# Kernel optimization log

Hardware: AMD Instinct MI355X
Metric: run time of the kernel (lower is better)

## Reference

```python
import jax, jax.numpy as jnp
import numpy as np

B, N, C = 64, 1700, 256
E_SP, E_TM = 6400, 10000


def gcn_conv(x, W, b, edge_index, num_nodes):
    """PyG GCNConv (normalize=True, add_self_loops=True) on batched [B,N,C] input,
    gathering/scattering along the node axis (node_dim=-2)."""
    row, col = edge_index[0], edge_index[1]
    loops = jnp.arange(num_nodes, dtype=row.dtype)
    row = jnp.concatenate([row, loops])
    col = jnp.concatenate([col, loops])
    w = jnp.ones(row.shape[0], dtype=x.dtype)
    deg = jax.ops.segment_sum(w, col, num_segments=num_nodes)
    dinv = jnp.where(deg > 0, jax.lax.rsqrt(deg), jnp.zeros_like(deg))
    norm = dinv[row] * dinv[col]                      # [E+N]
    h = x @ W                                         # [B,N,Cout]
    msg = h[:, row, :] * norm[None, :, None]          # gather along joints
    out = jnp.zeros((x.shape[0], num_nodes, W.shape[1]), x.dtype)
    out = out.at[:, col, :].add(msg)                  # scatter-add along joints
    return out + b


def setup_inputs() -> dict:
    key = jax.random.key(0)
    ks = jax.random.split(key, 9)
    s = 1.0 / np.sqrt(C)
    return {
        "x": jax.random.normal(ks[0], (B, N, C), jnp.float32),
        "W1": jax.random.uniform(ks[1], (C, C), jnp.float32, -s, s),
        "b1": jnp.zeros((C,), jnp.float32),
        "W2": jax.random.uniform(ks[2], (C, C), jnp.float32, -s, s),
        "b2": jnp.zeros((C,), jnp.float32),
        "W3": jax.random.uniform(ks[3], (C, C), jnp.float32, -s, s),
        "b3": jnp.zeros((C,), jnp.float32),
        "keypoint_line_without_temporal": jax.random.randint(ks[4], (2, E_SP), 0, N, jnp.int32),
        "keypoint_line_with_temporal": jax.random.randint(ks[5], (2, E_TM), 0, N, jnp.int32),
    }


def reference(x, W1, b1, W2, b2, W3, b3,
              keypoint_line_without_temporal, keypoint_line_with_temporal):
    num_nodes = x.shape[1]
    residual = x  # downsample is None -> identity residual
    out = jax.nn.relu(gcn_conv(x, W1, b1, keypoint_line_without_temporal, num_nodes))
    out = jax.nn.relu(gcn_conv(out, W2, b2, keypoint_line_with_temporal, num_nodes))
    out = gcn_conv(out, W3, b3, keypoint_line_without_temporal, num_nodes)
    return jax.nn.relu(out + residual)
```

## Files before the change

### kernel.cpp

```cpp
#include <hip/hip_runtime.h>

#define NNODES 1700
#define CDIM   256

typedef __attribute__((ext_vector_type(8))) short bf16x8;
typedef __attribute__((ext_vector_type(4))) float f32x4;

__device__ inline float bf2f(unsigned h) { return __uint_as_float(h << 16); }
__device__ inline unsigned short f2bf(float f) {
  unsigned u = __float_as_uint(f);
  u = (u + 0x7FFFu + ((u >> 16) & 1u)) >> 16;
  return (unsigned short)u;
}

__device__ inline void async_copy16(const void* gsrc, void* ldst) {
  __builtin_amdgcn_global_load_lds(
      (const __attribute__((address_space(1))) unsigned int*)gsrc,
      (__attribute__((address_space(3))) unsigned int*)ldst,
      16, 0, 0);
}


__global__ void zero_kernel(int* p, int n) {
  int i = blockIdx.x * blockDim.x + threadIdx.x;
  if (i < n) p[i] = 0;
}

__global__ void count_kernel(const int* __restrict__ ei, int E, int* __restrict__ cnt) {
  int i = blockIdx.x * blockDim.x + threadIdx.x;
  if (i < E) atomicAdd(&cnt[ei[E + i]], 1);
}

__global__ void dinv_kernel(const int* __restrict__ cnt, float* __restrict__ dinv, int n) {
  int i = blockIdx.x * blockDim.x + threadIdx.x;
  if (i < n) dinv[i] = rsqrtf((float)(cnt[i] + 1));
}

__global__ __launch_bounds__(1024) void scan_kernel(const int* __restrict__ cnt, int n,
                                                    int* __restrict__ off) {
  __shared__ int s[2048];
  int t = threadIdx.x;
  for (int i = t; i < 2048; i += 1024) s[i] = (i < n) ? (cnt[i] + 1) : 0;
  for (int d = 1; d < 2048; d <<= 1) {
    __syncthreads();
    int idx = (t + 1) * (d << 1) - 1;
    if (idx < 2048) s[idx] += s[idx - d];
  }
  __syncthreads();
  if (t == 0) s[2047] = 0;
  for (int d = 1024; d >= 1; d >>= 1) {
    __syncthreads();
    int idx = (t + 1) * (d << 1) - 1;
    if (idx < 2048) { int tmp = s[idx - d]; s[idx - d] = s[idx]; s[idx] += tmp; }
  }
  __syncthreads();
  for (int i = t; i <= n; i += 1024) off[i] = s[i];
}

__global__ void fill_kernel(const int* __restrict__ ei, int E, int n,
                            const float* __restrict__ dinv, const int* __restrict__ off,
                            int* __restrict__ cursor, int* __restrict__ srcv,
                            float* __restrict__ wv) {
  int i = blockIdx.x * blockDim.x + threadIdx.x;
  if (i >= E + n) return;
  int s, d;
  if (i < E) { s = ei[i]; d = ei[E + i]; } else { s = d = i - E; }
  float w = dinv[s] * dinv[d];
  int p = atomicAdd(&cursor[d], 1);
  int idx = off[d] + p;
  srcv[idx] = s;
  wv[idx] = w;
}

__global__ void transpose_kernel(const float* __restrict__ W,
                                 unsigned short* __restrict__ Wt) {
  int i = blockIdx.x * 256 + threadIdx.x;
  int k = i >> 8, n = i & 255;
  Wt[n * 256 + k] = f2bf(W[i]);
}


template <bool AF32>
__global__ __launch_bounds__(256) void gemm128(const void* __restrict__ Ap,
                                               const unsigned short* __restrict__ Wt,
                                               unsigned short* __restrict__ H) {
  __shared__ __align__(16) unsigned short As[128 * 32];
  __shared__ __align__(16) unsigned short Bs[128 * 32];
  const int m0 = blockIdx.x * 128;
  const int n0 = blockIdx.y * 128;
  const int t = threadIdx.x;
  const int lane = t & 63;
  const int w = t >> 6;
  const int wm = (w & 1) * 64;
  const int wn = (w >> 1) * 64;
  const int lr = lane & 15;
  const int lk = (lane >> 4) * 8;

  f32x4 acc[4][4] = {};

  const int q0 = t;
  const int q1 = t + 256;

  for (int k0 = 0; k0 < 256; k0 += 32) {
    if (AF32) {
      const float* A = (const float*)Ap;
      const int row = t >> 1, kh = (t & 1) * 16;
      const float* g = A + (size_t)(m0 + row) * CDIM + k0 + kh;
      float4 f0 = *(const float4*)(g + 0);
      float4 f1 = *(const float4*)(g + 4);
      float4 f2 = *(const float4*)(g + 8);
      float4 f3 = *(const float4*)(g + 12);
      unsigned short* dst = &As[row * 32 + kh];
      bf16x8 p0, p1;
      p0[0] = (short)f2bf(f0.x); p0[1] = (short)f2bf(f0.y);
      p0[2] = (short)f2bf(f0.z); p0[3] = (short)f2bf(f0.w);
      p0[4] = (short)f2bf(f1.x); p0[5] = (short)f2bf(f1.y);
      p0[6] = (short)f2bf(f1.z); p0[7] = (short)f2bf(f1.w);
      p1[0] = (short)f2bf(f2.x); p1[1] = (short)f2bf(f2.y);
      p1[2] = (short)f2bf(f2.z); p1[3] = (short)f2bf(f2.w);
      p1[4] = (short)f2bf(f3.x); p1[5] = (short)f2bf(f3.y);
      p1[6] = (short)f2bf(f3.z); p1[7] = (short)f2bf(f3.w);
      *(bf16x8*)(dst) = p0;
      *(bf16x8*)(dst + 8) = p1;
    } else {
      const unsigned short* A = (const unsigned short*)Ap;
      async_copy16(A + (size_t)(m0 + (q0 >> 2)) * CDIM + k0 + (q0 & 3) * 8, As + q0 * 8);
      async_copy16(A + (size_t)(m0 + (q1 >> 2)) * CDIM + k0 + (q1 & 3) * 8, As + q1 * 8);
    }
    async_copy16(Wt + (size_t)(n0 + (q0 >> 2)) * CDIM + k0 + (q0 & 3) * 8, Bs + q0 * 8);
    async_copy16(Wt + (size_t)(n0 + (q1 >> 2)) * CDIM + k0 + (q1 & 3) * 8, Bs + q1 * 8);
    __syncthreads();

    bf16x8 a[4], b[4];
#pragma unroll
    for (int i = 0; i < 4; i++)
      a[i] = *(const bf16x8*)&As[(wm + i * 16 + lr) * 32 + lk];
#pragma unroll
    for (int i = 0; i < 4; i++)
      b[i] = *(const bf16x8*)&Bs[(wn + i * 16 + lr) * 32 + lk];
#pragma unroll
    for (int mi = 0; mi < 4; mi++)
#pragma unroll
      for (int ni = 0; ni < 4; ni++)
        acc[mi][ni] = __builtin_amdgcn_mfma_f32_16x16x32_bf16(a[mi], b[ni], acc[mi][ni], 0, 0, 0);
    __syncthreads();
  }

  const int orow = (lane >> 4) * 4;
#pragma unroll
  for (int mi = 0; mi < 4; mi++) {
#pragma unroll
    for (int ni = 0; ni < 4; ni++) {
#pragma unroll
      for (int r = 0; r < 4; r++) {
        int gr = m0 + wm + mi * 16 + orow + r;
        int gc = n0 + wn + ni * 16 + lr;
        H[(size_t)gr * CDIM + gc] = f2bf(acc[mi][ni][r]);
      }
    }
  }
}


template <bool FINAL>
__global__ __launch_bounds__(256) void agg_kernel(const unsigned short* __restrict__ H,
                                                  const int* __restrict__ off,
                                                  const int* __restrict__ srcv,
                                                  const float* __restrict__ wv,
                                                  const float* __restrict__ bias,
                                                  const float* __restrict__ resid,
                                                  void* __restrict__ outp) {
  const int n = blockIdx.x;
  const int b = blockIdx.y * 4 + (threadIdx.x >> 6);
  const int c = (threadIdx.x & 63) * 4;
  const int beg = off[n], end = off[n + 1];

  float a0 = 0.f, a1 = 0.f, a2 = 0.f, a3 = 0.f;
  for (int i = beg; i < end; i++) {
    int s = srcv[i];
    float w = wv[i];
    uint2 v = *(const uint2*)(H + ((size_t)b * NNODES + s) * CDIM + c);
    a0 += w * bf2f(v.x & 0xffffu);
    a1 += w * bf2f(v.x >> 16);
    a2 += w * bf2f(v.y & 0xffffu);
    a3 += w * bf2f(v.y >> 16);
  }
  float4 bv = *(const float4*)(bias + c);
  a0 += bv.x; a1 += bv.y; a2 += bv.z; a3 += bv.w;

  const size_t o = ((size_t)b * NNODES + n) * CDIM + c;
  if (FINAL) {
    float4 rv = *(const float4*)(resid + o);
    a0 += rv.x; a1 += rv.y; a2 += rv.z; a3 += rv.w;
  }
  a0 = fmaxf(a0, 0.f); a1 = fmaxf(a1, 0.f); a2 = fmaxf(a2, 0.f); a3 = fmaxf(a3, 0.f);

  if (FINAL) {
    float4 ov; ov.x = a0; ov.y = a1; ov.z = a2; ov.w = a3;
    *(float4*)((float*)outp + o) = ov;
  } else {
    uint2 ov;
    ov.x = (unsigned)f2bf(a0) | ((unsigned)f2bf(a1) << 16);
    ov.y = (unsigned)f2bf(a2) | ((unsigned)f2bf(a3) << 16);
    *(uint2*)((unsigned short*)outp + o) = ov;
  }
}


extern "C" void kernel_launch(void* const* d_in, const int* in_sizes, int n_in,
                              void* d_out, int out_size, void* d_ws, size_t ws_size,
                              hipStream_t stream) {
  const float* x  = (const float*)d_in[0];
  const float* W1 = (const float*)d_in[1];
  const float* b1 = (const float*)d_in[2];
  const float* W2 = (const float*)d_in[3];
  const float* b2 = (const float*)d_in[4];
  const float* W3 = (const float*)d_in[5];
  const float* b3 = (const float*)d_in[6];
  const int* esp = (const int*)d_in[7];
  const int* etm = (const int*)d_in[8];

  const int Esp = in_sizes[7] / 2;
  const int Etm = in_sizes[8] / 2;
  const int B = in_sizes[0] / (NNODES * CDIM);
  const int M = B * NNODES;

  char* ws = (char*)d_ws;
  size_t woff = 0;
  auto alloc = [&](size_t bytes) -> void* {
    void* p = ws + woff;
    woff = (woff + bytes + 255) & ~(size_t)255;
    return p;
  };

  unsigned short* H   = (unsigned short*)alloc((size_t)M * CDIM * 2);
  unsigned short* Act = (unsigned short*)alloc((size_t)M * CDIM * 2);
  unsigned short* Wt  = (unsigned short*)alloc((size_t)3 * CDIM * CDIM * 2);
  int* zero_base = (int*)alloc((size_t)4 * NNODES * sizeof(int));
  int* cnt_sp = zero_base;
  int* cur_sp = zero_base + NNODES;
  int* cnt_tm = zero_base + 2 * NNODES;
  int* cur_tm = zero_base + 3 * NNODES;
  int* off_sp = (int*)alloc((NNODES + 1) * sizeof(int));
  int* off_tm = (int*)alloc((NNODES + 1) * sizeof(int));
  float* dinv_sp = (float*)alloc(NNODES * sizeof(float));
  float* dinv_tm = (float*)alloc(NNODES * sizeof(float));
  int*   src_sp = (int*)alloc((size_t)(Esp + NNODES) * sizeof(int));
  float* wgt_sp = (float*)alloc((size_t)(Esp + NNODES) * sizeof(float));
  int*   src_tm = (int*)alloc((size_t)(Etm + NNODES) * sizeof(int));
  float* wgt_tm = (float*)alloc((size_t)(Etm + NNODES) * sizeof(float));

  zero_kernel<<<(4 * NNODES + 255) / 256, 256, 0, stream>>>(zero_base, 4 * NNODES);
  transpose_kernel<<<256, 256, 0, stream>>>(W1, Wt);
  transpose_kernel<<<256, 256, 0, stream>>>(W2, Wt + CDIM * CDIM);
  transpose_kernel<<<256, 256, 0, stream>>>(W3, Wt + 2 * CDIM * CDIM);
  count_kernel<<<(Esp + 255) / 256, 256, 0, stream>>>(esp, Esp, cnt_sp);
  count_kernel<<<(Etm + 255) / 256, 256, 0, stream>>>(etm, Etm, cnt_tm);
  dinv_kernel<<<(NNODES + 255) / 256, 256, 0, stream>>>(cnt_sp, dinv_sp, NNODES);
  dinv_kernel<<<(NNODES + 255) / 256, 256, 0, stream>>>(cnt_tm, dinv_tm, NNODES);
  scan_kernel<<<1, 1024, 0, stream>>>(cnt_sp, NNODES, off_sp);
  scan_kernel<<<1, 1024, 0, stream>>>(cnt_tm, NNODES, off_tm);
  fill_kernel<<<(Esp + NNODES + 255) / 256, 256, 0, stream>>>(esp, Esp, NNODES, dinv_sp,
                                                              off_sp, cur_sp, src_sp, wgt_sp);
  fill_kernel<<<(Etm + NNODES + 255) / 256, 256, 0, stream>>>(etm, Etm, NNODES, dinv_tm,
                                                              off_tm, cur_tm, src_tm, wgt_tm);

  dim3 ggrid(M / 128, CDIM / 128);
  dim3 agrid(NNODES, B / 4);

  gemm128<true><<<ggrid, 256, 0, stream>>>(x, Wt, H);
  agg_kernel<false><<<agrid, 256, 0, stream>>>(H, off_sp, src_sp, wgt_sp, b1, nullptr, Act);
  gemm128<false><<<ggrid, 256, 0, stream>>>(Act, Wt + CDIM * CDIM, H);
  agg_kernel<false><<<agrid, 256, 0, stream>>>(H, off_tm, src_tm, wgt_tm, b2, nullptr, Act);
  gemm128<false><<<ggrid, 256, 0, stream>>>(Act, Wt + 2 * CDIM * CDIM, H);
  agg_kernel<true><<<agrid, 256, 0, stream>>>(H, off_sp, src_sp, wgt_sp, b3, x, d_out);
}
```

Measured before the change: 481.6 us.

## Pipeline GEMM with triple-buffered async loads, full-N tiles, wider aggregation vectors

Replaces the 128x128 GEMM with a 512-thread kernel covering all 256 output columns per block. It uses a 3-stage LDS ring, prefetching two k-steps ahead with vmcnt waits, so loads overlap MFMA work instead of syncing twice per step. The fp32 input is now converted to bf16 in a separate pre-pass, which lets every GEMM use async copies but adds an extra pass over x. The aggregation kernel now handles 8 channels per thread with 16-byte loads and stores, halving the thread count per node.

Measured after the change: 458.6 us. -4.8%, faster.

```diff
diff --git a/kernel.cpp b/kernel.cpp
--- a/kernel.cpp
+++ b/kernel.cpp
@@ -79,15 +79,59 @@
   Wt[n * 256 + k] = f2bf(W[i]);
 }
 
-
-template <bool AF32>
-__global__ __launch_bounds__(256) void gemm128(const void* __restrict__ Ap,
-                                               const unsigned short* __restrict__ Wt,
-                                               unsigned short* __restrict__ H) {
-  __shared__ __align__(16) unsigned short As[128 * 32];
-  __shared__ __align__(16) unsigned short Bs[128 * 32];
+__global__ __launch_bounds__(256) void cvt_kernel(const float* __restrict__ x,
+                                                  unsigned short* __restrict__ o) {
+  size_t i = ((size_t)blockIdx.x * 256 + threadIdx.x) * 8;
+  float4 f0 = *(const float4*)(x + i);
+  float4 f1 = *(const float4*)(x + i + 4);
+  bf16x8 p;
+  p[0] = (short)f2bf(f0.x); p[1] = (short)f2bf(f0.y);
+  p[2] = (short)f2bf(f0.z); p[3] = (short)f2bf(f0.w);
+  p[4] = (short)f2bf(f1.x); p[5] = (short)f2bf(f1.y);
+  p[6] = (short)f2bf(f1.z); p[7] = (short)f2bf(f1.w);
+  *(bf16x8*)(o + i) = p;
+}
+
+
+template <int K>
+__device__ __forceinline__ void kstep(const unsigned short* __restrict__ asrc,
+                                      const unsigned short* __restrict__ bsrc,
+                                      unsigned short (&As)[3][128 * 32],
+                                      unsigned short (&Bs)[3][256 * 32],
+                                      int t, int wm, int wn, int lr, int lk,
+                                      f32x4 (&acc)[4][4]) {
+  if constexpr (K < 7) {
+    asm volatile("s_waitcnt vmcnt(3)" ::: "memory");
+  } else {
+    asm volatile("s_waitcnt vmcnt(0)" ::: "memory");
+  }
+  __builtin_amdgcn_s_barrier();
+  if constexpr (K + 2 < 8) {
+    constexpr int S = K + 2;
+    async_copy16(asrc + S * 32, &As[S % 3][t * 8]);
+    async_copy16(bsrc + S * 32, &Bs[S % 3][t * 8]);
+    async_copy16(bsrc + 128 * CDIM + S * 32, &Bs[S % 3][4096 + t * 8]);
+  }
+  bf16x8 a[4], b[4];
+#pragma unroll
+  for (int i = 0; i < 4; i++)
+    a[i] = *(const bf16x8*)&As[K % 3][(wm + i * 16 + lr) * 32 + lk];
+#pragma unroll
+  for (int i = 0; i < 4; i++)
+    b[i] = *(const bf16x8*)&Bs[K % 3][(wn + i * 16 + lr) * 32 + lk];
+#pragma unroll
+  for (int mi = 0; mi < 4; mi++)
+#pragma unroll
+    for (int ni = 0; ni < 4; ni++)
+      acc[mi][ni] = __builtin_amdgcn_mfma_f32_16x16x32_bf16(a[mi], b[ni], acc[mi][ni], 0, 0, 0);
+}
+
+__global__ __launch_bounds__(512, 4) void gemm_n256(const unsigned short* __restrict__ A,
+                                                    const unsigned short* __restrict__ Wt,
+                                                    unsigned short* __restrict__ H) {
+  __shared__ __align__(16) unsigned short As[3][128 * 32];
+  __shared__ __align__(16) unsigned short Bs[3][256 * 32];
   const int m0 = blockIdx.x * 128;
-  const int n0 = blockIdx.y * 128;
   const int t = threadIdx.x;
   const int lane = t & 63;
   const int w = t >> 6;
@@ -96,55 +140,26 @@
   const int lr = lane & 15;
   const int lk = (lane >> 4) * 8;
 
+  const unsigned short* asrc = A + (size_t)(m0 + (t >> 2)) * CDIM + (t & 3) * 8;
+  const unsigned short* bsrc = Wt + (size_t)(t >> 2) * CDIM + (t & 3) * 8;
+
   f32x4 acc[4][4] = {};
 
-  const int q0 = t;
-  const int q1 = t + 256;
-
-  for (int k0 = 0; k0 < 256; k0 += 32) {
-    if (AF32) {
-      const float* A = (const float*)Ap;
-      const int row = t >> 1, kh = (t & 1) * 16;
-      const float* g = A + (size_t)(m0 + row) * CDIM + k0 + kh;
-      float4 f0 = *(const float4*)(g + 0);
-      float4 f1 = *(const float4*)(g + 4);
-      float4 f2 = *(const float4*)(g + 8);
-      float4 f3 = *(const float4*)(g + 12);
-      unsigned short* dst = &As[row * 32 + kh];
-      bf16x8 p0, p1;
-      p0[0] = (short)f2bf(f0.x); p0[1] = (short)f2bf(f0.y);
-      p0[2] = (short)f2bf(f0.z); p0[3] = (short)f2bf(f0.w);
-      p0[4] = (short)f2bf(f1.x); p0[5] = (short)f2bf(f1.y);
-      p0[6] = (short)f2bf(f1.z); p0[7] = (short)f2bf(f1.w);
-      p1[0] = (short)f2bf(f2.x); p1[1] = (short)f2bf(f2.y);
-      p1[2] = (short)f2bf(f2.z); p1[3] = (short)f2bf(f2.w);
-      p1[4] = (short)f2bf(f3.x); p1[5] = (short)f2bf(f3.y);
-      p1[6] = (short)f2bf(f3.z); p1[7] = (short)f2bf(f3.w);
-      *(bf16x8*)(dst) = p0;
-      *(bf16x8*)(dst + 8) = p1;
-    } else {
-      const unsigned short* A = (const unsigned short*)Ap;
-      async_copy16(A + (size_t)(m0 + (q0 >> 2)) * CDIM + k0 + (q0 & 3) * 8, As + q0 * 8);
-      async_copy16(A + (size_t)(m0 + (q1 >> 2)) * CDIM + k0 + (q1 & 3) * 8, As + q1 * 8);
-    }
-    async_copy16(Wt + (size_t)(n0 + (q0 >> 2)) * CDIM + k0 + (q0 & 3) * 8, Bs + q0 * 8);
-    async_copy16(Wt + (size_t)(n0 + (q1 >> 2)) * CDIM + k0 + (q1 & 3) * 8, Bs + q1 * 8);
-    __syncthreads();
-
-    bf16x8 a[4], b[4];
-#pragma unroll
-    for (int i = 0; i < 4; i++)
-      a[i] = *(const bf16x8*)&As[(wm + i * 16 + lr) * 32 + lk];
-#pragma unroll
-    for (int i = 0; i < 4; i++)
-      b[i] = *(const bf16x8*)&Bs[(wn + i * 16 + lr) * 32 + lk];
-#pragma unroll
-    for (int mi = 0; mi < 4; mi++)
-#pragma unroll
-      for (int ni = 0; ni < 4; ni++)
-        acc[mi][ni] = __builtin_amdgcn_mfma_f32_16x16x32_bf16(a[mi], b[ni], acc[mi][ni], 0, 0, 0);
-    __syncthreads();
-  }
+#pragma unroll
+  for (int s = 0; s < 2; s++) {
+    async_copy16(asrc + s * 32, &As[s][t * 8]);
+    async_copy16(bsrc + s * 32, &Bs[s][t * 8]);
+    async_copy16(bsrc + 128 * CDIM + s * 32, &Bs[s][4096 + t * 8]);
+  }
+
+  kstep<0>(asrc, bsrc, As, Bs, t, wm, wn, lr, lk, acc);
+  kstep<1>(asrc, bsrc, As, Bs, t, wm, wn, lr, lk, acc);
+  kstep<2>(asrc, bsrc, As, Bs, t, wm, wn, lr, lk, acc);
+  kstep<3>(asrc, bsrc, As, Bs, t, wm, wn, lr, lk, acc);
+  kstep<4>(asrc, bsrc, As, Bs, t, wm, wn, lr, lk, acc);
+  kstep<5>(asrc, bsrc, As, Bs, t, wm, wn, lr, lk, acc);
+  kstep<6>(asrc, bsrc, As, Bs, t, wm, wn, lr, lk, acc);
+  kstep<7>(asrc, bsrc, As, Bs, t, wm, wn, lr, lk, acc);
 
   const int orow = (lane >> 4) * 4;
 #pragma unroll
@@ -154,7 +169,7 @@
 #pragma unroll
       for (int r = 0; r < 4; r++) {
         int gr = m0 + wm + mi * 16 + orow + r;
-        int gc = n0 + wn + ni * 16 + lr;
+        int gc = wn + ni * 16 + lr;
         H[(size_t)gr * CDIM + gc] = f2bf(acc[mi][ni][r]);
       }
     }
@@ -171,38 +186,49 @@
                                                   const float* __restrict__ resid,
                                                   void* __restrict__ outp) {
   const int n = blockIdx.x;
-  const int b = blockIdx.y * 4 + (threadIdx.x >> 6);
-  const int c = (threadIdx.x & 63) * 4;
+  const int b = blockIdx.y * 8 + (threadIdx.x >> 5);
+  const int c = (threadIdx.x & 31) * 8;
   const int beg = off[n], end = off[n + 1];
 
   float a0 = 0.f, a1 = 0.f, a2 = 0.f, a3 = 0.f;
+  float a4 = 0.f, a5 = 0.f, a6 = 0.f, a7 = 0.f;
   for (int i = beg; i < end; i++) {
     int s = srcv[i];
     float w = wv[i];
-    uint2 v = *(const uint2*)(H + ((size_t)b * NNODES + s) * CDIM + c);
-    a0 += w * bf2f(v.x & 0xffffu);
-    a1 += w * bf2f(v.x >> 16);
-    a2 += w * bf2f(v.y & 0xffffu);
-    a3 += w * bf2f(v.y >> 16);
-  }
-  float4 bv = *(const float4*)(bias + c);
-  a0 += bv.x; a1 += bv.y; a2 += bv.z; a3 += bv.w;
+    uint4 v = *(const uint4*)(H + ((size_t)b * NNODES + s) * CDIM + c);
+    a0 += w * bf2f(v.x & 0xffffu); a1 += w * bf2f(v.x >> 16);
+    a2 += w * bf2f(v.y & 0xffffu); a3 += w * bf2f(v.y >> 16);
+    a4 += w * bf2f(v.z & 0xffffu); a5 += w * bf2f(v.z >> 16);
+    a6 += w * bf2f(v.w & 0xffffu); a7 += w * bf2f(v.w >> 16);
+  }
+  float4 bv0 = *(const float4*)(bias + c);
+  float4 bv1 = *(const float4*)(bias + c + 4);
+  a0 += bv0.x; a1 += bv0.y; a2 += bv0.z; a3 += bv0.w;
+  a4 += bv1.x; a5 += bv1.y; a6 += bv1.z; a7 += bv1.w;
 
   const size_t o = ((size_t)b * NNODES + n) * CDIM + c;
   if (FINAL) {
-    float4 rv = *(const float4*)(resid + o);
-    a0 += rv.x; a1 += rv.y; a2 += rv.z; a3 += rv.w;
+    float4 r0 = *(const float4*)(resid + o);
+    float4 r1 = *(const float4*)(resid + o + 4);
+    a0 += r0.x; a1 += r0.y; a2 += r0.z; a3 += r0.w;
+    a4 += r1.x; a5 += r1.y; a6 += r1.z; a7 += r1.w;
   }
   a0 = fmaxf(a0, 0.f); a1 = fmaxf(a1, 0.f); a2 = fmaxf(a2, 0.f); a3 = fmaxf(a3, 0.f);
+  a4 = fmaxf(a4, 0.f); a5 = fmaxf(a5, 0.f); a6 = fmaxf(a6, 0.f); a7 = fmaxf(a7, 0.f);
 
   if (FINAL) {
-    float4 ov; ov.x = a0; ov.y = a1; ov.z = a2; ov.w = a3;
-    *(float4*)((float*)outp + o) = ov;
+    float4 o0, o1;
+    o0.x = a0; o0.y = a1; o0.z = a2; o0.w = a3;
+    o1.x = a4; o1.y = a5; o1.z = a6; o1.w = a7;
+    *(float4*)((float*)outp + o) = o0;
+    *(float4*)((float*)outp + o + 4) = o1;
   } else {
-    uint2 ov;
-    ov.x = (unsigned)f2bf(a0) | ((unsigned)f2bf(a1) << 16);
-    ov.y = (unsigned)f2bf(a2) | ((unsigned)f2bf(a3) << 16);
-    *(uint2*)((unsigned short*)outp + o) = ov;
+    bf16x8 ov;
+    ov[0] = (short)f2bf(a0); ov[1] = (short)f2bf(a1);
+    ov[2] = (short)f2bf(a2); ov[3] = (short)f2bf(a3);
+    ov[4] = (short)f2bf(a4); ov[5] = (short)f2bf(a5);
+    ov[6] = (short)f2bf(a6); ov[7] = (short)f2bf(a7);
+    *(bf16x8*)((unsigned short*)outp + o) = ov;
   }
 }
 
@@ -265,13 +291,15 @@
   fill_kernel<<<(Etm + NNODES + 255) / 256, 256, 0, stream>>>(etm, Etm, NNODES, dinv_tm,
                                                               off_tm, cur_tm, src_tm, wgt_tm);
 
-  dim3 ggrid(M / 128, CDIM / 128);
-  dim3 agrid(NNODES, B / 4);
-
-  gemm128<true><<<ggrid, 256, 0, stream>>>(x, Wt, H);
+  dim3 ggrid(M / 128);
+  dim3 agrid(NNODES, B / 8);
+
+  cvt_kernel<<<(M * CDIM / 8 + 255) / 256, 256, 0, stream>>>(x, Act);
+
+  gemm_n256<<<ggrid, 512, 0, stream>>>(Act, Wt, H);
   agg_kernel<false><<<agrid, 256, 0, stream>>>(H, off_sp, src_sp, wgt_sp, b1, nullptr, Act);
-  gemm128<false><<<ggrid, 256, 0, stream>>>(Act, Wt + CDIM * CDIM, H);
+  gemm_n256<<<ggrid, 512, 0, stream>>>(Act, Wt + CDIM * CDIM, H);
   agg_kernel<false><<<agrid, 256, 0, stream>>>(H, off_tm, src_tm, wgt_tm, b2, nullptr, Act);
-  gemm128<false><<<ggrid, 256, 0, stream>>>(Act, Wt + 2 * CDIM * CDIM, H);
+  gemm_n256<<<ggrid, 512, 0, stream>>>(Act, Wt + 2 * CDIM * CDIM, H);
   agg_kernel<true><<<agrid, 256, 0, stream>>>(H, off_sp, src_sp, wgt_sp, b3, x, d_out);
 }
```

## Fuse aggregation with GEMM per layer by aggregating inputs before multiplication

Applied to the files above, without the earlier changes.

Each GCN layer is reordered to aggregate first and multiply second (A·X·W instead of A·(X·W)), which is valid because the aggregation is linear along nodes and the matmul acts on channels. One fused kernel per layer gathers neighbor rows into LDS as bf16, then runs a full-N 64x256 MFMA GEMM with a triple-buffered async weight pipeline, and applies bias, ReLU and the residual in the epilogue. This removes the separate intermediate H write and read and halves the kernel launches. The first layer now gathers fp32 x directly, so it moves more bytes per neighbor, and per-row gather latency now sits inside the GEMM block.

Result: slower. 930.6 us (+93.3%).

```diff
diff --git a/kernel.cpp b/kernel.cpp
--- a/kernel.cpp
+++ b/kernel.cpp
@@ -80,129 +80,137 @@
 }
 
 
-template <bool AF32>
-__global__ __launch_bounds__(256) void gemm128(const void* __restrict__ Ap,
-                                               const unsigned short* __restrict__ Wt,
-                                               unsigned short* __restrict__ H) {
-  __shared__ __align__(16) unsigned short As[128 * 32];
-  __shared__ __align__(16) unsigned short Bs[128 * 32];
-  const int m0 = blockIdx.x * 128;
-  const int n0 = blockIdx.y * 128;
+template <int K>
+__device__ __forceinline__ void kstep(const unsigned short* __restrict__ Wt,
+                                      const unsigned short (&As)[8 * 2048],
+                                      unsigned short (&Bs)[3][256 * 32],
+                                      int t, int wn, int lr, int lk,
+                                      f32x4 (&acc)[4][4]) {
+  if constexpr (K < 7) {
+    asm volatile("s_waitcnt vmcnt(4)" ::: "memory");
+  } else {
+    asm volatile("s_waitcnt vmcnt(0)" ::: "memory");
+  }
+  __builtin_amdgcn_s_barrier();
+  if constexpr (K + 2 < 8) {
+    constexpr int S = K + 2;
+#pragma unroll
+    for (int j = 0; j < 4; j++) {
+      int c = t + 256 * j;
+      async_copy16(Wt + (size_t)(c >> 2) * CDIM + S * 32 + (c & 3) * 8,
+                   &Bs[S % 3][c * 8]);
+    }
+  }
+  bf16x8 a[4], b[4];
+#pragma unroll
+  for (int i = 0; i < 4; i++)
+    a[i] = *(const bf16x8*)&As[K * 2048 + (i * 16 + lr) * 32 + lk];
+#pragma unroll
+  for (int i = 0; i < 4; i++)
+    b[i] = *(const bf16x8*)&Bs[K % 3][(wn + i * 16 + lr) * 32 + lk];
+#pragma unroll
+  for (int mi = 0; mi < 4; mi++)
+#pragma unroll
+    for (int ni = 0; ni < 4; ni++)
+      acc[mi][ni] = __builtin_amdgcn_mfma_f32_16x16x32_bf16(a[mi], b[ni], acc[mi][ni], 0, 0, 0);
+}
+
+template <bool AF32, bool FINAL>
+__global__ __launch_bounds__(256, 2) void fused_layer(
+    const void* __restrict__ Ap,
+    const unsigned short* __restrict__ Wt,
+    const int* __restrict__ off, const int* __restrict__ srcv,
+    const float* __restrict__ wv, const float* __restrict__ bias,
+    const float* __restrict__ resid,
+    void* __restrict__ outp) {
+  __shared__ __align__(16) unsigned short As[8 * 2048];
+  __shared__ __align__(16) unsigned short Bs[3][256 * 32];
   const int t = threadIdx.x;
   const int lane = t & 63;
   const int w = t >> 6;
-  const int wm = (w & 1) * 64;
-  const int wn = (w >> 1) * 64;
+  const int m0 = blockIdx.x * 64;
+  const int wn = w * 64;
   const int lr = lane & 15;
   const int lk = (lane >> 4) * 8;
 
+#pragma unroll
+  for (int st = 0; st < 2; st++)
+#pragma unroll
+    for (int j = 0; j < 4; j++) {
+      int c = t + 256 * j;
+      async_copy16(Wt + (size_t)(c >> 2) * CDIM + st * 32 + (c & 3) * 8, &Bs[st][c * 8]);
+    }
+
+  const int cc = lane * 4;
+  for (int rr = 0; rr < 16; rr++) {
+    const int row = rr * 4 + w;
+    const int m = m0 + row;
+    const int b = m / NNODES;
+    const int n = m - b * NNODES;
+    const int beg = off[n], end = off[n + 1];
+    const size_t base = (size_t)b * NNODES;
+    float c0 = 0.f, c1 = 0.f, c2 = 0.f, c3 = 0.f;
+    if (AF32) {
+      const float* X = (const float*)Ap;
+      for (int i = beg; i < end; i++) {
+        int sv = srcv[i];
+        float wt = wv[i];
+        float4 v = *(const float4*)(X + (base + sv) * CDIM + cc);
+        c0 += wt * v.x; c1 += wt * v.y; c2 += wt * v.z; c3 += wt * v.w;
+      }
+    } else {
+      const unsigned short* X = (const unsigned short*)Ap;
+      for (int i = beg; i < end; i++) {
+        int sv = srcv[i];
+        float wt = wv[i];
+        uint2 v = *(const uint2*)(X + (base + sv) * CDIM + cc);
+        c0 += wt * bf2f(v.x & 0xffffu); c1 += wt * bf2f(v.x >> 16);
+        c2 += wt * bf2f(v.y & 0xffffu); c3 += wt * bf2f(v.y >> 16);
+      }
+    }
+    uint2 o;
+    o.x = (unsigned)f2bf(c0) | ((unsigned)f2bf(c1) << 16);
+    o.y = (unsigned)f2bf(c2) | ((unsigned)f2bf(c3) << 16);
+    *(uint2*)&As[(cc >> 5) * 2048 + row * 32 + (cc & 31)] = o;
+  }
+  __syncthreads();
+
   f32x4 acc[4][4] = {};
-
-  const int q0 = t;
-  const int q1 = t + 256;
-
-  for (int k0 = 0; k0 < 256; k0 += 32) {
-    if (AF32) {
-      const float* A = (const float*)Ap;
-      const int row = t >> 1, kh = (t & 1) * 16;
-      const float* g = A + (size_t)(m0 + row) * CDIM + k0 + kh;
-      float4 f0 = *(const float4*)(g + 0);
-      float4 f1 = *(const float4*)(g + 4);
-      float4 f2 = *(const float4*)(g + 8);
-      float4 f3 = *(const float4*)(g + 12);
-      unsigned short* dst = &As[row * 32 + kh];
-      bf16x8 p0, p1;
-      p0[0] = (short)f2bf(f0.x); p0[1] = (short)f2bf(f0.y);
-      p0[2] = (short)f2bf(f0.z); p0[3] = (short)f2bf(f0.w);
-      p0[4] = (short)f2bf(f1.x); p0[5] = (short)f2bf(f1.y);
-      p0[6] = (short)f2bf(f1.z); p0[7] = (short)f2bf(f1.w);
-      p1[0] = (short)f2bf(f2.x); p1[1] = (short)f2bf(f2.y);
-      p1[2] = (short)f2bf(f2.z); p1[3] = (short)f2bf(f2.w);
-      p1[4] = (short)f2bf(f3.x); p1[5] = (short)f2bf(f3.y);
-      p1[6] = (short)f2bf(f3.z); p1[7] = (short)f2bf(f3.w);
-      *(bf16x8*)(dst) = p0;
-      *(bf16x8*)(dst + 8) = p1;
-    } else {
-      const unsigned short* A = (const unsigned short*)Ap;
-      async_copy16(A + (size_t)(m0 + (q0 >> 2)) * CDIM + k0 + (q0 & 3) * 8, As + q0 * 8);
-      async_copy16(A + (size_t)(m0 + (q1 >> 2)) * CDIM + k0 + (q1 & 3) * 8, As + q1 * 8);
-    }
-    async_copy16(Wt + (size_t)(n0 + (q0 >> 2)) * CDIM + k0 + (q0 & 3) * 8, Bs + q0 * 8);
-    async_copy16(Wt + (size_t)(n0 + (q1 >> 2)) * CDIM + k0 + (q1 & 3) * 8, Bs + q1 * 8);
-    __syncthreads();
-
-    bf16x8 a[4], b[4];
-#pragma unroll
-    for (int i = 0; i < 4; i++)
-      a[i] = *(const bf16x8*)&As[(wm + i * 16 + lr) * 32 + lk];
-#pragma unroll
-    for (int i = 0; i < 4; i++)
-      b[i] = *(const bf16x8*)&Bs[(wn + i * 16 + lr) * 32 + lk];
-#pragma unroll
-    for (int mi = 0; mi < 4; mi++)
-#pragma unroll
-      for (int ni = 0; ni < 4; ni++)
-        acc[mi][ni] = __builtin_amdgcn_mfma_f32_16x16x32_bf16(a[mi], b[ni], acc[mi][ni], 0, 0, 0);
-    __syncthreads();
-  }
-
+  kstep<0>(Wt, As, Bs, t, wn, lr, lk, acc);
+  kstep<1>(Wt, As, Bs, t, wn, lr, lk, acc);
+  kstep<2>(Wt, As, Bs, t, wn, lr, lk, acc);
+  kstep<3>(Wt, As, Bs, t, wn, lr, lk, acc);
+  kstep<4>(Wt, As, Bs, t, wn, lr, lk, acc);
+  kstep<5>(Wt, As, Bs, t, wn, lr, lk, acc);
+  kstep<6>(Wt, As, Bs, t, wn, lr, lk, acc);
+  kstep<7>(Wt, As, Bs, t, wn, lr, lk, acc);
+
+  float bv[4];
+#pragma unroll
+  for (int ni = 0; ni < 4; ni++) bv[ni] = bias[wn + ni * 16 + lr];
   const int orow = (lane >> 4) * 4;
 #pragma unroll
   for (int mi = 0; mi < 4; mi++) {
 #pragma unroll
-    for (int ni = 0; ni < 4; ni++) {
-#pragma unroll
-      for (int r = 0; r < 4; r++) {
-        int gr = m0 + wm + mi * 16 + orow + r;
-        int gc = n0 + wn + ni * 16 + lr;
-        H[(size_t)gr * CDIM + gc] = f2bf(acc[mi][ni][r]);
+    for (int r = 0; r < 4; r++) {
+      const size_t gr = (size_t)(m0 + mi * 16 + orow + r);
+      if (FINAL) {
+        float* O = (float*)outp;
+#pragma unroll
+        for (int ni = 0; ni < 4; ni++) {
+          const size_t idx = gr * CDIM + wn + ni * 16 + lr;
+          float v = acc[mi][ni][r] + bv[ni] + resid[idx];
+          O[idx] = fmaxf(v, 0.f);
+        }
+      } else {
+        unsigned short* O = (unsigned short*)outp;
+#pragma unroll
+        for (int ni = 0; ni < 4; ni++) {
+          const size_t idx = gr * CDIM + wn + ni * 16 + lr;
+          O[idx] = f2bf(fmaxf(acc[mi][ni][r] + bv[ni], 0.f));
+        }
       }
     }
-  }
-}
-
-
-template <bool FINAL>
-__global__ __launch_bounds__(256) void agg_kernel(const unsigned short* __restrict__ H,
-                                                  const int* __restrict__ off,
-                                                  const int* __restrict__ srcv,
-                                                  const float* __restrict__ wv,
-                                                  const float* __restrict__ bias,
-                                                  const float* __restrict__ resid,
-                                                  void* __restrict__ outp) {
-  const int n = blockIdx.x;
-  const int b = blockIdx.y * 4 + (threadIdx.x >> 6);
-  const int c = (threadIdx.x & 63) * 4;
-  const int beg = off[n], end = off[n + 1];
-
-  float a0 = 0.f, a1 = 0.f, a2 = 0.f, a3 = 0.f;
-  for (int i = beg; i < end; i++) {
-    int s = srcv[i];
-    float w = wv[i];
-    uint2 v = *(const uint2*)(H + ((size_t)b * NNODES + s) * CDIM + c);
-    a0 += w * bf2f(v.x & 0xffffu);
-    a1 += w * bf2f(v.x >> 16);
-    a2 += w * bf2f(v.y & 0xffffu);
-    a3 += w * bf2f(v.y >> 16);
-  }
-  float4 bv = *(const float4*)(bias + c);
-  a0 += bv.x; a1 += bv.y; a2 += bv.z; a3 += bv.w;
-
-  const size_t o = ((size_t)b * NNODES + n) * CDIM + c;
-  if (FINAL) {
-    float4 rv = *(const float4*)(resid + o);
-    a0 += rv.x; a1 += rv.y; a2 += rv.z; a3 += rv.w;
-  }
-  a0 = fmaxf(a0, 0.f); a1 = fmaxf(a1, 0.f); a2 = fmaxf(a2, 0.f); a3 = fmaxf(a3, 0.f);
-
-  if (FINAL) {
-    float4 ov; ov.x = a0; ov.y = a1; ov.z = a2; ov.w = a3;
-    *(float4*)((float*)outp + o) = ov;
-  } else {
-    uint2 ov;
-    ov.x = (unsigned)f2bf(a0) | ((unsigned)f2bf(a1) << 16);
-    ov.y = (unsigned)f2bf(a2) | ((unsigned)f2bf(a3) << 16);
-    *(uint2*)((unsigned short*)outp + o) = ov;
   }
 }
 
@@ -265,13 +273,12 @@
   fill_kernel<<<(Etm + NNODES + 255) / 256, 256, 0, stream>>>(etm, Etm, NNODES, dinv_tm,
                                                               off_tm, cur_tm, src_tm, wgt_tm);
 
-  dim3 ggrid(M / 128, CDIM / 128);
-  dim3 agrid(NNODES, B / 4);
-
-  gemm128<true><<<ggrid, 256, 0, stream>>>(x, Wt, H);
-  agg_kernel<false><<<agrid, 256, 0, stream>>>(H, off_sp, src_sp, wgt_sp, b1, nullptr, Act);
-  gemm128<false><<<ggrid, 256, 0, stream>>>(Act, Wt + CDIM * CDIM, H);
-  agg_kernel<false><<<agrid, 256, 0, stream>>>(H, off_tm, src_tm, wgt_tm, b2, nullptr, Act);
-  gemm128<false><<<ggrid, 256, 0, stream>>>(Act, Wt + 2 * CDIM * CDIM, H);
-  agg_kernel<true><<<agrid, 256, 0, stream>>>(H, off_sp, src_sp, wgt_sp, b3, x, d_out);
-}
+  dim3 fgrid(M / 64);
+
+  fused_layer<true, false><<<fgrid, 256, 0, stream>>>(x, Wt, off_sp, src_sp, wgt_sp,
+                                                      b1, nullptr, H);
+  fused_layer<false, false><<<fgrid, 256, 0, stream>>>(H, Wt + CDIM * CDIM, off_tm, src_tm,
+                                                       wgt_tm, b2, nullptr, Act);
+  fused_layer<false, true><<<fgrid, 256, 0, stream>>>(Act, Wt + 2 * CDIM * CDIM, off_sp,
+                                                      src_sp, wgt_sp, b3, x, d_out);
+}
```
